# Kernel optimization log

Measured on AMD Instinct MI355X. Metric: run time of the kernel, lower is better.

The kernel has to match this reference:

```python
import jax, jax.numpy as jnp
import numpy as np

N = 50000    # nodes
E = 800000   # edges (avg degree 16)
B = 256      # graphs in the batch (static for segment ops)
H = 128      # feature / hidden width (channels[-2])
NL = 4       # LSTM layers in Set2Set
PS = 4       # Set2Set processing steps
OUT = 2      # channels[-1]


def _bn(h, g, b):
    # BatchNorm1d with batch statistics (training-mode math, biased variance)
    m = h.mean(0)
    v = jnp.mean((h - m) ** 2, 0)
    return (h - m) * jax.lax.rsqrt(v + 1e-5) * g + b


def _gin(x, src, dst, W1, b1, ga1, be1, W2, b2, ga2, be2):
    # GINConv, eps=0: out = MLP(x + sum_{j->i} x_j)
    agg = jax.ops.segment_sum(x[src], dst, num_segments=x.shape[0])
    h = x + agg
    h = jax.nn.relu(_bn(h @ W1.T + b1, ga1, be1))
    h = jax.nn.relu(_bn(h @ W2.T + b2, ga2, be2))
    return h


def _set2set(x, batch, Wih0, Whh0, b0, WihR, WhhR, bR):
    hs = [jnp.zeros((B, H), x.dtype)] * NL
    cs = [jnp.zeros((B, H), x.dtype)] * NL
    q_star = jnp.zeros((B, 2 * H), x.dtype)
    for _ in range(PS):
        inp = q_star
        nhs, ncs = [], []
        for l in range(NL):  # stacked LSTM cells, seq-len 1 per step
            Wih = Wih0 if l == 0 else WihR[l - 1]
            Whh = Whh0 if l == 0 else WhhR[l - 1]
            bb = b0 if l == 0 else bR[l - 1]
            gates = inp @ Wih.T + hs[l] @ Whh.T + bb
            i, f, g, o = jnp.split(gates, 4, axis=-1)  # torch gate order i,f,g,o
            c = jax.nn.sigmoid(f) * cs[l] + jax.nn.sigmoid(i) * jnp.tanh(g)
            h = jax.nn.sigmoid(o) * jnp.tanh(c)
            nhs.append(h); ncs.append(c)
            inp = h
        hs, cs = nhs, ncs
        q = inp  # (B, H) top-layer hidden
        # per-graph segment softmax attention
        e = jnp.sum(x * q[batch], -1)                        # (N,)
        m = jax.ops.segment_max(e, batch, num_segments=B)
        ee = jnp.exp(e - m[batch])
        s = jax.ops.segment_sum(ee, batch, num_segments=B)
        a = ee / s[batch]
        r = jax.ops.segment_sum(a[:, None] * x, batch, num_segments=B)  # (B, H)
        q_star = jnp.concatenate([q, r], -1)
    return q_star


def setup_inputs() -> dict:
    key = jax.random.key(0)
    ks = jax.random.split(key, 16)

    def w(k, shape):
        return jax.random.normal(k, shape, jnp.float32) * 0.05

    d = {}
    d["x"] = jax.random.normal(ks[0], (N, H), jnp.float32)
    d["edge_index"] = jax.random.randint(ks[1], (2, E), 0, N, dtype=jnp.int32)
    d["batch"] = jnp.sort(jax.random.randint(ks[2], (N,), 0, B, dtype=jnp.int32))
    for i, g in enumerate(("g0", "g1")):
        kk = jax.random.split(ks[3 + i], 2)
        d[g + "_W1"] = w(kk[0], (H, H)); d[g + "_b1"] = jnp.zeros((H,), jnp.float32)
        d[g + "_gamma1"] = jnp.ones((H,), jnp.float32); d[g + "_beta1"] = jnp.zeros((H,), jnp.float32)
        d[g + "_W2"] = w(kk[1], (H, H)); d[g + "_b2"] = jnp.zeros((H,), jnp.float32)
        d[g + "_gamma2"] = jnp.ones((H,), jnp.float32); d[g + "_beta2"] = jnp.zeros((H,), jnp.float32)
    d["Wih0"] = w(ks[6], (4 * H, 2 * H))
    d["Whh0"] = w(ks[7], (4 * H, H))
    d["b0"] = jnp.zeros((4 * H,), jnp.float32)
    d["WihR"] = w(ks[8], (NL - 1, 4 * H, H))
    d["WhhR"] = w(ks[9], (NL - 1, 4 * H, H))
    d["bR"] = jnp.zeros((NL - 1, 4 * H), jnp.float32)
    d["lin_W"] = w(ks[10], (OUT, 2 * H))
    d["lin_b"] = jnp.zeros((OUT,), jnp.float32)
    return d


def reference(x, edge_index, batch,
              g0_W1, g0_b1, g0_gamma1, g0_beta1, g0_W2, g0_b2, g0_gamma2, g0_beta2,
              g1_W1, g1_b1, g1_gamma1, g1_beta1, g1_W2, g1_b2, g1_gamma2, g1_beta2,
              Wih0, Whh0, b0, WihR, WhhR, bR, lin_W, lin_b):
    src, dst = edge_index[0], edge_index[1]
    x = _gin(x, src, dst, g0_W1, g0_b1, g0_gamma1, g0_beta1, g0_W2, g0_b2, g0_gamma2, g0_beta2)
    x = _gin(x, src, dst, g1_W1, g1_b1, g1_gamma1, g1_beta1, g1_W2, g1_b2, g1_gamma2, g1_beta2)
    q = _set2set(x, batch, Wih0, Whh0, b0, WihR, WhhR, bR)
    # F.dropout(p=0.1) is identity in eval mode
    return q @ lin_W.T + lin_b
```

## Files before the change

### kernel.cpp

```cpp
#include <hip/hip_runtime.h>
#include <math.h>

#define NN 50000
#define EE 800000
#define BBG 256
#define HHC 128
#define SEG_CAP 448
#define ESC 512
#define NBIN 196
#define NBLK 196

typedef _Float16 half8 __attribute__((ext_vector_type(8)));
typedef _Float16 half4 __attribute__((ext_vector_type(4)));
typedef _Float16 half2v __attribute__((ext_vector_type(2)));
typedef float f32x4 __attribute__((ext_vector_type(4)));

#if defined(__has_builtin)
#if __has_builtin(__builtin_amdgcn_fdot2)
#define USE_FDOT2 1
#endif
#endif

__device__ __forceinline__ float fdot2f(half2v a, half2v b, float c) {
#ifdef USE_FDOT2
  return __builtin_amdgcn_fdot2(a, b, c, false);
#else
  return fmaf((float)a[0], (float)b[0], fmaf((float)a[1], (float)b[1], c));
#endif
}

__device__ __forceinline__ float fsigm(float x) {
  return __builtin_amdgcn_rcpf(1.f + __expf(-x));
}
__device__ __forceinline__ float ftanh(float x) {
  return 1.f - 2.f * __builtin_amdgcn_rcpf(1.f + __expf(2.f * x));
}

__device__ __forceinline__ float4 aff4(float4 v, float4 sc, float4 sh) {
  v.x = fmaxf(fmaf(v.x, sc.x, sh.x), 0.f);
  v.y = fmaxf(fmaf(v.y, sc.y, sh.y), 0.f);
  v.z = fmaxf(fmaf(v.z, sc.z, sh.z), 0.f);
  v.w = fmaxf(fmaf(v.w, sc.w, sh.w), 0.f);
  return v;
}
__device__ __forceinline__ void add4(float4& a, float4 b) {
  a.x += b.x; a.y += b.y; a.z += b.z; a.w += b.w;
}
__device__ __forceinline__ float4 cvt4(half4 h) {
  return make_float4((float)h[0], (float)h[1], (float)h[2], (float)h[3]);
}

__global__ __launch_bounds__(256) void prep_all_kernel(
    const int* __restrict__ batch,
    const int* __restrict__ ei,
    const float* __restrict__ W0, const float* __restrict__ W1,
    const float* __restrict__ W2, const float* __restrict__ W3,
    const float* __restrict__ Wih0, const float* __restrict__ Whh0,
    const float* __restrict__ WihR, const float* __restrict__ WhhR,
    const float* __restrict__ b0, const float* __restrict__ bR,
    const float* __restrict__ xsrc,
    float* __restrict__ stats, int* __restrict__ gptr, int* __restrict__ partial,
    _Float16* __restrict__ ginWh, _Float16* __restrict__ WT0h,
    _Float16* __restrict__ WTRh, float* __restrict__ bc0, float* __restrict__ bcR,
    _Float16* __restrict__ x16a) {
  __shared__ int hist[NBIN];
  int blk = blockIdx.x, tid = threadIdx.x;
  if (blk == 0) {
    ((float4*)stats)[tid] = make_float4(0.f, 0.f, 0.f, 0.f);
    return;
  }
  if (blk <= 196) {
    int i = (blk - 1) * 256 + tid;
    if (i >= NN) return;
    int b = batch[i];
    int prev = (i == 0) ? -1 : batch[i - 1];
    for (int g = prev + 1; g <= b; ++g) gptr[g] = i;
    if (i == NN - 1) {
      for (int g = b + 1; g <= BBG; ++g) gptr[g] = NN;
    }
    return;
  }
  if (blk <= 392) {
    int b = blk - 197;
    if (tid < NBIN) hist[tid] = 0;
    __syncthreads();
    const int4* dst4 = (const int4*)(ei + EE);
#pragma unroll
    for (int c = 0; c < 4; ++c) {
      int idx = b * 1024 + c * 256 + tid;
      if (idx < EE / 4) {
        int4 d = dst4[idx];
        atomicAdd(&hist[d.x >> 8], 1);
        atomicAdd(&hist[d.y >> 8], 1);
        atomicAdd(&hist[d.z >> 8], 1);
        atomicAdd(&hist[d.w >> 8], 1);
      }
    }
    __syncthreads();
    if (tid < NBIN) partial[tid * NBLK + b] = hist[tid];
    return;
  }
  if (blk >= 2961) {
    int i = (blk - 2961) * 256 + tid;
    float4 v = ((const float4*)xsrc)[i];
    half4 h;
    h[0] = (_Float16)v.x; h[1] = (_Float16)v.y;
    h[2] = (_Float16)v.z; h[3] = (_Float16)v.w;
    ((half4*)x16a)[i] = h;
    return;
  }
  int idx = (blk - 393) * 256 + tid;
  if (idx < 65536) {
    int m = idx >> 14;
    int r = idx & 16383;
    const float* W = (m == 0) ? W0 : (m == 1) ? W1 : (m == 2) ? W2 : W3;
    ginWh[idx] = (_Float16)W[r];
  } else if (idx < 262144) {
    int t = idx - 65536;
    int k = t >> 9, op = t & 511;
    int j = op >> 2, g = op & 3;
    int row = g * 128 + j;
    float v = (k < 256) ? Wih0[row * 256 + k] : Whh0[row * 128 + (k - 256)];
    WT0h[((k >> 1) << 10) | (op << 1) | (k & 1)] = (_Float16)v;
  } else if (idx < 655360) {
    int t = idx - 262144;
    int l = t >> 17;
    int rem = t & 131071;
    int k = rem >> 9, op = rem & 511;
    int j = op >> 2, g = op & 3;
    int row = g * 128 + j;
    float v = (k < 128) ? WihR[((size_t)l * 512 + row) * 128 + k]
                        : WhhR[((size_t)l * 512 + row) * 128 + (k - 128)];
    WTRh[((size_t)l << 17) | ((k >> 1) << 10) | (op << 1) | (k & 1)] = (_Float16)v;
  } else {
    int t = idx - 655360;
    if (t < 512) {
      bc0[t] = b0[(t & 3) * 128 + (t >> 2)];
    } else {
      int u = t - 512;
      int l = u >> 9, op = u & 511;
      bcR[u] = bR[l * 512 + (op & 3) * 128 + (op >> 2)];
    }
  }
}


__global__ void scan_partials_kernel(const int* __restrict__ partial,
                                     int* __restrict__ block_base, int* __restrict__ total) {
  __shared__ int buf[256];
  int bin = blockIdx.x, tid = threadIdx.x;
  int v = (tid < NBLK) ? partial[bin * NBLK + tid] : 0;
  buf[tid] = v;
  __syncthreads();
  for (int off = 1; off < 256; off <<= 1) {
    int t = (tid >= off) ? buf[tid - off] : 0;
    __syncthreads();
    buf[tid] += t;
    __syncthreads();
  }
  if (tid < NBLK) block_base[bin * NBLK + tid] = buf[tid] - v;
  if (tid == 255) total[bin] = buf[255];
}

__global__ void scan_totals_kernel(const int* __restrict__ total, int* __restrict__ coarse_base) {
  __shared__ int buf[256];
  int tid = threadIdx.x;
  int v = (tid < NBIN) ? total[tid] : 0;
  buf[tid] = v;
  __syncthreads();
  for (int off = 1; off < 256; off <<= 1) {
    int t = (tid >= off) ? buf[tid - off] : 0;
    __syncthreads();
    buf[tid] += t;
    __syncthreads();
  }
  if (tid < NBIN) coarse_base[tid] = buf[tid] - v;
  if (tid == 255) coarse_base[NBIN] = buf[255];
}

__global__ __launch_bounds__(256) void bucket_scatter_kernel(const int* __restrict__ ei,
                                                             const int* __restrict__ coarse_base,
                                                             const int* __restrict__ block_base,
                                                             int* __restrict__ packed) {
  __shared__ int cursor[NBIN];
  int tid = threadIdx.x, b = blockIdx.x;
  if (tid < NBIN) cursor[tid] = coarse_base[tid] + block_base[tid * NBLK + b];
  __syncthreads();
  const int4* src4 = (const int4*)ei;
  const int4* dst4 = (const int4*)(ei + EE);
#pragma unroll
  for (int c = 0; c < 4; ++c) {
    int idx = b * 1024 + c * 256 + tid;
    if (idx < EE / 4) {
      int4 s = src4[idx];
      int4 d = dst4[idx];
      int p;
      p = atomicAdd(&cursor[d.x >> 8], 1); packed[p] = (s.x << 8) | (d.x & 255);
      p = atomicAdd(&cursor[d.y >> 8], 1); packed[p] = (s.y << 8) | (d.y & 255);
      p = atomicAdd(&cursor[d.z >> 8], 1); packed[p] = (s.z << 8) | (d.z & 255);
      p = atomicAdd(&cursor[d.w >> 8], 1); packed[p] = (s.w << 8) | (d.w & 255);
    }
  }
}

__global__ __launch_bounds__(256) void csr_finalize_kernel(const int* __restrict__ packed,
                                                           const int* __restrict__ coarse_base,
                                                           int* __restrict__ row_start,
                                                           int* __restrict__ csr) {
  __shared__ int fh[256];
  __shared__ int fb[256];
  int bin = blockIdx.x, tid = threadIdx.x;
  int e0 = coarse_base[bin], e1 = coarse_base[bin + 1];
  fh[tid] = 0;
  __syncthreads();
  for (int e = e0 + tid; e < e1; e += 256) atomicAdd(&fh[packed[e] & 255], 1);
  __syncthreads();
  int v = fh[tid];
  fb[tid] = v;
  __syncthreads();
  for (int off = 1; off < 256; off <<= 1) {
    int t = (tid >= off) ? fb[tid - off] : 0;
    __syncthreads();
    fb[tid] += t;
    __syncthreads();
  }
  int excl = fb[tid] - v;
  int node = bin * 256 + tid;
  if (node < NN) row_start[node] = e0 + excl;
  if (bin == NBIN - 1 && tid == 0) row_start[NN] = EE;
  __syncthreads();
  fb[tid] = excl;
  __syncthreads();
  for (int e = e0 + tid; e < e1; e += 256) {
    int p = packed[e];
    int pos = atomicAdd(&fb[p & 255], 1);
    csr[e0 + pos] = p >> 8;
  }
}


template <bool AFF>
__global__ __launch_bounds__(256) void gin_agg_kernel(
    const _Float16* __restrict__ x16, const int* __restrict__ row_start,
    const int* __restrict__ csr,
    const float* __restrict__ stats, const float* __restrict__ gamma,
    const float* __restrict__ beta, float* __restrict__ outp) {
  __shared__ float sc_s[128], sh_s[128];
  if (AFF) {
    int t = threadIdx.x;
    if (t < 128) {
      const float invN = 1.0f / (float)NN;
      float mm = stats[t] * invN;
      float vv = stats[128 + t] * invN - mm * mm;
      float rs = rsqrtf(vv + 1e-5f);
      float sc = gamma[t] * rs;
      sc_s[t] = sc;
      sh_s[t] = beta[t] - mm * sc;
    }
    __syncthreads();
  }
  int node = blockIdx.x * 4 + (threadIdx.x >> 6);
  int lane = threadIdx.x & 63;
  int half = lane >> 5, ln = lane & 31;
  const half4* xh = (const half4*)x16;
  float4 sc4 = make_float4(0.f, 0.f, 0.f, 0.f), sh4 = sc4;
  if (AFF) {
    sc4 = *(const float4*)&sc_s[4 * ln];
    sh4 = *(const float4*)&sh_s[4 * ln];
  }
  int s0 = row_start[node], s1 = row_start[node + 1];
  float4 self = cvt4(xh[(size_t)node * 32 + ln]);
  if (AFF) self = aff4(self, sc4, sh4);
  float4 c0 = make_float4(0.f, 0.f, 0.f, 0.f), c1 = c0, c2 = c0, c3 = c0;
  int cnt = s1 - s0;
  int mainEnd = s0 + (cnt & ~15);
  for (int j = s0; j < mainEnd; j += 16) {
    int i0 = csr[j + half + 0];
    int i1 = csr[j + half + 2];
    int i2 = csr[j + half + 4];
    int i3 = csr[j + half + 6];
    int i4 = csr[j + half + 8];
    int i5 = csr[j + half + 10];
    int i6 = csr[j + half + 12];
    int i7 = csr[j + half + 14];
    half4 h0 = xh[(size_t)i0 * 32 + ln];
    half4 h1 = xh[(size_t)i1 * 32 + ln];
    half4 h2 = xh[(size_t)i2 * 32 + ln];
    half4 h3 = xh[(size_t)i3 * 32 + ln];
    half4 h4 = xh[(size_t)i4 * 32 + ln];
    half4 h5 = xh[(size_t)i5 * 32 + ln];
    half4 h6 = xh[(size_t)i6 * 32 + ln];
    half4 h7 = xh[(size_t)i7 * 32 + ln];
    float4 v0 = cvt4(h0);
    float4 v1 = cvt4(h1);
    float4 v2 = cvt4(h2);
    float4 v3 = cvt4(h3);
    float4 v4 = cvt4(h4);
    float4 v5 = cvt4(h5);
    float4 v6 = cvt4(h6);
    float4 v7 = cvt4(h7);
    if (AFF) {
      v0 = aff4(v0, sc4, sh4); v1 = aff4(v1, sc4, sh4);
      v2 = aff4(v2, sc4, sh4); v3 = aff4(v3, sc4, sh4);
      v4 = aff4(v4, sc4, sh4); v5 = aff4(v5, sc4, sh4);
      v6 = aff4(v6, sc4, sh4); v7 = aff4(v7, sc4, sh4);
    }
    add4(c0, v0); add4(c1, v1); add4(c2, v2); add4(c3, v3);
    add4(c0, v4); add4(c1, v5); add4(c2, v6); add4(c3, v7);
  }
  for (int j = mainEnd + half; j < s1; j += 2) {
    int i = csr[j];
    float4 v = cvt4(xh[(size_t)i * 32 + ln]);
    if (AFF) v = aff4(v, sc4, sh4);
    add4(c0, v);
  }
  float4 t;
  t.x = (c0.x + c1.x) + (c2.x + c3.x);
  t.y = (c0.y + c1.y) + (c2.y + c3.y);
  t.z = (c0.z + c1.z) + (c2.z + c3.z);
  t.w = (c0.w + c1.w) + (c2.w + c3.w);
  t.x += __shfl_xor(t.x, 32);
  t.y += __shfl_xor(t.y, 32);
  t.z += __shfl_xor(t.z, 32);
  t.w += __shfl_xor(t.w, 32);
  t.x += self.x; t.y += self.y; t.z += self.z; t.w += self.w;
  if (half == 0) ((float4*)outp)[(size_t)node * 32 + ln] = t;
}

template <bool BN, bool AH>
__global__ __launch_bounds__(256) void gemm_gin_mfma_kernel(
    const float* __restrict__ A, const _Float16* __restrict__ A16,
    const _Float16* __restrict__ Wh,
    const float* __restrict__ bias,
    const float* __restrict__ stats, const float* __restrict__ gamma,
    const float* __restrict__ beta,
    float* __restrict__ C, _Float16* __restrict__ h16out,
    float* __restrict__ ssum, float* __restrict__ ssq) {
  __shared__ float bsc_s[128], bsh_s[128];
  int tid = threadIdx.x;
  if (BN) {
    if (tid < 128) {
      const float invN = 1.0f / (float)NN;
      float mm = stats[tid] * invN;
      float vv = stats[128 + tid] * invN - mm * mm;
      float rs = rsqrtf(vv + 1e-5f);
      float sc = gamma[tid] * rs;
      bsc_s[tid] = sc;
      bsh_s[tid] = beta[tid] - mm * sc;
    }
    __syncthreads();
  }
  int w = tid >> 6, l = tid & 63;
  int lr = l & 15, lg = l >> 4;
  int cb = w * 32;
  half8 bf0[4], bf1[4];
#pragma unroll
  for (int ks = 0; ks < 4; ++ks) {
    int k = ks * 32 + lg * 8;
    bf0[ks] = *(const half8*)(Wh + (size_t)(cb + lr) * 128 + k);
    bf1[ks] = *(const half8*)(Wh + (size_t)(cb + 16 + lr) * 128 + k);
  }
  float bv0 = bias[cb + lr], bv1 = bias[cb + 16 + lr];
  float ps0 = 0.f, pq0 = 0.f, ps1 = 0.f, pq1 = 0.f;
  int t0 = blockIdx.x * 4;
  for (int t = 0; t < 4; ++t) {
    int tile = t0 + t;
    if (tile >= 3125) break;
    int r = tile * 16 + lr;
    half8 af[4];
#pragma unroll
    for (int ks = 0; ks < 4; ++ks) {
      int k0 = ks * 32 + lg * 8;
      if constexpr (AH) {
        half8 ah = *(const half8*)(A16 + (size_t)r * 128 + k0);
        if constexpr (BN) {
          float4 s0 = *(const float4*)&bsc_s[k0];
          float4 s1 = *(const float4*)&bsc_s[k0 + 4];
          float4 h0 = *(const float4*)&bsh_s[k0];
          float4 h1 = *(const float4*)&bsh_s[k0 + 4];
          half8 o;
          o[0] = (_Float16)fmaxf(fmaf((float)ah[0], s0.x, h0.x), 0.f);
          o[1] = (_Float16)fmaxf(fmaf((float)ah[1], s0.y, h0.y), 0.f);
          o[2] = (_Float16)fmaxf(fmaf((float)ah[2], s0.z, h0.z), 0.f);
          o[3] = (_Float16)fmaxf(fmaf((float)ah[3], s0.w, h0.w), 0.f);
          o[4] = (_Float16)fmaxf(fmaf((float)ah[4], s1.x, h1.x), 0.f);
          o[5] = (_Float16)fmaxf(fmaf((float)ah[5], s1.y, h1.y), 0.f);
          o[6] = (_Float16)fmaxf(fmaf((float)ah[6], s1.z, h1.z), 0.f);
          o[7] = (_Float16)fmaxf(fmaf((float)ah[7], s1.w, h1.w), 0.f);
          af[ks] = o;
        } else {
          af[ks] = ah;
        }
      } else {
        float4 a0 = *(const float4*)(A + (size_t)r * 128 + k0);
        float4 a1 = *(const float4*)(A + (size_t)r * 128 + k0 + 4);
        if constexpr (BN) {
          float4 s0 = *(const float4*)&bsc_s[k0];
          float4 s1 = *(const float4*)&bsc_s[k0 + 4];
          float4 h0 = *(const float4*)&bsh_s[k0];
          float4 h1 = *(const float4*)&bsh_s[k0 + 4];
          a0 = aff4(a0, s0, h0);
          a1 = aff4(a1, s1, h1);
        }
        half8 o;
        o[0] = (_Float16)a0.x; o[1] = (_Float16)a0.y;
        o[2] = (_Float16)a0.z; o[3] = (_Float16)a0.w;
        o[4] = (_Float16)a1.x; o[5] = (_Float16)a1.y;
        o[6] = (_Float16)a1.z; o[7] = (_Float16)a1.w;
        af[ks] = o;
      }
    }
    f32x4 acc0 = {0.f, 0.f, 0.f, 0.f};
    f32x4 acc1 = {0.f, 0.f, 0.f, 0.f};
#pragma unroll
    for (int ks = 0; ks < 4; ++ks) {
      acc0 = __builtin_amdgcn_mfma_f32_16x16x32_f16(af[ks], bf0[ks], acc0, 0, 0, 0);
      acc1 = __builtin_amdgcn_mfma_f32_16x16x32_f16(af[ks], bf1[ks], acc1, 0, 0, 0);
    }
#pragma unroll
    for (int i = 0; i < 4; ++i) {
      int rr = tile * 16 + lg * 4 + i;
      float v0 = acc0[i] + bv0;
      float v1 = acc1[i] + bv1;
      if (C) {
        C[(size_t)rr * 128 + cb + lr] = v0;
        C[(size_t)rr * 128 + cb + 16 + lr] = v1;
      }
      if (h16out) {
        h16out[(size_t)rr * 128 + cb + lr] = (_Float16)v0;
        h16out[(size_t)rr * 128 + cb + 16 + lr] = (_Float16)v1;
      }
      ps0 += v0; pq0 += v0 * v0;
      ps1 += v1; pq1 += v1 * v1;
    }
  }
  ps0 += __shfl_xor(ps0, 16); ps0 += __shfl_xor(ps0, 32);
  pq0 += __shfl_xor(pq0, 16); pq0 += __shfl_xor(pq0, 32);
  ps1 += __shfl_xor(ps1, 16); ps1 += __shfl_xor(ps1, 32);
  pq1 += __shfl_xor(pq1, 16); pq1 += __shfl_xor(pq1, 32);
  if (lg == 0) {
    atomicAdd(&ssum[cb + lr], ps0);
    atomicAdd(&ssq[cb + lr], pq0);
    atomicAdd(&ssum[cb + 16 + lr], ps1);
    atomicAdd(&ssq[cb + 16 + lr], pq1);
  }
}

__global__ void __launch_bounds__(1024) set2set_kernel(
    const float* __restrict__ x, const int* __restrict__ gptr,
    const float* __restrict__ stats, const float* __restrict__ gamma,
    const float* __restrict__ beta,
    const _Float16* __restrict__ WT0h, const _Float16* __restrict__ WTRh,
    const float* __restrict__ bc0, const float* __restrict__ bcR,
    float* __restrict__ ebuf,
    const float* __restrict__ linW, const float* __restrict__ linb,
    float* __restrict__ out) {
  __shared__ half2v xs[SEG_CAP * 64];
  __shared__ float wpart[16][512];
  __shared__ float gates[512];
  __shared__ half2v inp2[192];
  __shared__ float hcs[4][128];
  __shared__ float ccs[4][128];
  __shared__ float qst[256];
  __shared__ float es[ESC];
  __shared__ float bsc[128], bsh[128];
  __shared__ float wred[16];
  __shared__ float smax_s, ssum_s;
  __shared__ float fred[2][4];

  int g = blockIdx.x, tid = threadIdx.x;
  int w16 = tid >> 6, lane = tid & 63;

  if (tid < 128) {
    const float invN = 1.0f / (float)NN;
    float mm = stats[tid] * invN;
    float vv = stats[128 + tid] * invN - mm * mm;
    float rs = rsqrtf(vv + 1e-5f);
    float sc = gamma[tid] * rs;
    bsc[tid] = sc;
    bsh[tid] = beta[tid] - mm * sc;
#pragma unroll
    for (int l = 0; l < 4; ++l) { hcs[l][tid] = 0.f; ccs[l][tid] = 0.f; }
  }
  if (tid < 256) qst[tid] = 0.f;
  __syncthreads();

  int s0 = gptr[g], s1 = gptr[g + 1];
  int seg = s1 - s0;
  int ncache = seg < SEG_CAP ? seg : SEG_CAP;
  const float2* x2 = (const float2*)x;
  float sc0 = bsc[2 * lane], sc1 = bsc[2 * lane + 1];
  float sh0 = bsh[2 * lane], sh1 = bsh[2 * lane + 1];
  for (int n = w16; n < ncache; n += 16) {
    float2 v = x2[(size_t)(s0 + n) * 64 + lane];
    half2v h;
    h[0] = (_Float16)fmaxf(fmaf(v.x, sc0, sh0), 0.f);
    h[1] = (_Float16)fmaxf(fmaf(v.y, sc1, sh1), 0.f);
    xs[n * 64 + lane] = h;
  }
  __syncthreads();

  int s_ = tid >> 6, cg = tid & 63;

  for (int step = 0; step < 4; ++step) {
    for (int cell = 0; cell < 4; ++cell) {
      const _Float16* WTh; const float* bias; int KP2;
      if (cell == 0) {
        WTh = WT0h; bias = bc0; KP2 = 12;
        if (tid < 192) {
          int k = tid << 1;
          float va, vb;
          if (k < 256) { va = qst[k]; vb = qst[k + 1]; }
          else { va = hcs[0][k - 256]; vb = hcs[0][k - 255]; }
          half2v h; h[0] = (_Float16)va; h[1] = (_Float16)vb;
          inp2[tid] = h;
        }
      } else {
        WTh = WTRh + (size_t)(cell - 1) * 131072;
        bias = bcR + (cell - 1) * 512; KP2 = 8;
        if (tid < 128) {
          int k = tid << 1;
          float va, vb;
          if (k < 128) { va = hcs[cell - 1][k]; vb = hcs[cell - 1][k + 1]; }
          else { va = hcs[cell][k - 128]; vb = hcs[cell][k - 127]; }
          half2v h; h[0] = (_Float16)va; h[1] = (_Float16)vb;
          inp2[tid] = h;
        }
      }
      __syncthreads();
      if (step == 0 && cell == 0) {
        if (tid < 512) gates[tid] = bias[tid];
        __syncthreads();
      } else {
        int se = (s_ + g) & 15;
        int k20 = se * KP2;
        float a0 = 0.f, a1 = 0.f, a2 = 0.f, a3 = 0.f;
        float a4 = 0.f, a5 = 0.f, a6 = 0.f, a7 = 0.f;
        if (step != 0 || se < 8) {
          const char* wb = (const char*)WTh + (size_t)k20 * 2048 + (cg << 5);
#pragma unroll 4
          for (int k2 = 0; k2 < KP2; ++k2) {
            uint4 wa = *(const uint4*)(wb + (size_t)k2 * 2048);
            uint4 wc = *(const uint4*)(wb + (size_t)k2 * 2048 + 16);
            half2v i2 = inp2[k20 + k2];
            a0 = fdot2f(i2, __builtin_bit_cast(half2v, wa.x), a0);
            a1 = fdot2f(i2, __builtin_bit_cast(half2v, wa.y), a1);
            a2 = fdot2f(i2, __builtin_bit_cast(half2v, wa.z), a2);
            a3 = fdot2f(i2, __builtin_bit_cast(half2v, wa.w), a3);
            a4 = fdot2f(i2, __builtin_bit_cast(half2v, wc.x), a4);
            a5 = fdot2f(i2, __builtin_bit_cast(half2v, wc.y), a5);
            a6 = fdot2f(i2, __builtin_bit_cast(half2v, wc.z), a6);
            a7 = fdot2f(i2, __builtin_bit_cast(half2v, wc.w), a7);
          }
        }
        *(float4*)&wpart[s_][cg << 3] = make_float4(a0, a1, a2, a3);
        *(float4*)(&wpart[s_][cg << 3] + 4) = make_float4(a4, a5, a6, a7);
        __syncthreads();
        if (tid < 512) {
          float acc = bias[tid];
#pragma unroll
          for (int s = 0; s < 16; ++s) acc += wpart[s][tid];
          gates[tid] = acc;
        }
        __syncthreads();
      }
      if (tid < 128) {
        int j = tid;
        float gi = gates[4 * j + 0];
        float gf = gates[4 * j + 1];
        float gc = gates[4 * j + 2];
        float go = gates[4 * j + 3];
        float cp = ccs[cell][j];
        float si = fsigm(gi);
        float sf = fsigm(gf);
        float so = fsigm(go);
        float cn = sf * cp + si * ftanh(gc);
        ccs[cell][j] = cn;
        hcs[cell][j] = so * ftanh(cn);
      }
      __syncthreads();
    }
    float* rpart = &wpart[0][0];
    float qx = hcs[3][2 * lane], qy = hcs[3][2 * lane + 1];
    half2v q2; q2[0] = (_Float16)qx; q2[1] = (_Float16)qy;
    float wmax = -3.0e38f;
    for (int n = w16; n < seg; n += 16) {
      float e;
      if (n < ncache) {
        e = fdot2f(xs[n * 64 + lane], q2, 0.f);
      } else {
        float2 v = x2[(size_t)(s0 + n) * 64 + lane];
        float vx = fmaxf(fmaf(v.x, sc0, sh0), 0.f);
        float vy = fmaxf(fmaf(v.y, sc1, sh1), 0.f);
        e = vx * qx + vy * qy;
      }
#pragma unroll
      for (int sh = 32; sh; sh >>= 1) e += __shfl_xor(e, sh);
      if (lane == 0) { if (n < ESC) es[n] = e; else ebuf[s0 + n] = e; }
      wmax = fmaxf(wmax, e);
    }
    if (lane == 0) wred[w16] = wmax;
    __syncthreads();
    if (tid == 0) {
      float m = wred[0];
#pragma unroll
      for (int t = 1; t < 16; ++t) m = fmaxf(m, wred[t]);
      smax_s = m;
    }
    __syncthreads();
    float m = smax_s;
    float loc = 0.f;
    for (int n = tid; n < seg; n += 1024) {
      float e = (n < ESC) ? es[n] : ebuf[s0 + n];
      float ex = __expf(e - m);
      if (n < ESC) es[n] = ex; else ebuf[s0 + n] = ex;
      loc += ex;
    }
#pragma unroll
    for (int sh = 32; sh; sh >>= 1) loc += __shfl_xor(loc, sh);
    __syncthreads();
    if (lane == 0) wred[w16] = loc;
    __syncthreads();
    if (tid == 0) {
      float s = 0.f;
#pragma unroll
      for (int t = 0; t < 16; ++t) s += wred[t];
      ssum_s = s;
    }
    __syncthreads();
    float inv = 1.0f / ssum_s;
    float rx = 0.f, ry = 0.f;
    for (int n = w16; n < seg; n += 16) {
      float ex = (n < ESC) ? es[n] : ebuf[s0 + n];
      float coef = ex * inv;
      float vx, vy;
      if (n < ncache) {
        half2v v2 = xs[n * 64 + lane];
        vx = (float)v2[0]; vy = (float)v2[1];
      } else {
        float2 v = x2[(size_t)(s0 + n) * 64 + lane];
        vx = fmaxf(fmaf(v.x, sc0, sh0), 0.f);
        vy = fmaxf(fmaf(v.y, sc1, sh1), 0.f);
      }
      rx += coef * vx; ry += coef * vy;
    }
    rpart[w16 * 128 + 2 * lane] = rx;
    rpart[w16 * 128 + 2 * lane + 1] = ry;
    __syncthreads();
    if (tid < 128) {
      float r = 0.f;
#pragma unroll
      for (int t = 0; t < 16; ++t) r += rpart[t * 128 + tid];
      qst[tid] = hcs[3][tid];
      qst[128 + tid] = r;
    }
    __syncthreads();
  }
  if (tid < 256) {
    float val = qst[tid];
    float p0 = val * linW[tid];
    float p1 = val * linW[256 + tid];
#pragma unroll
    for (int sh = 32; sh; sh >>= 1) { p0 += __shfl_xor(p0, sh); p1 += __shfl_xor(p1, sh); }
    if (lane == 0) { fred[0][w16] = p0; fred[1][w16] = p1; }
  }
  __syncthreads();
  if (tid == 0) {
    out[2 * g + 0] = fred[0][0] + fred[0][1] + fred[0][2] + fred[0][3] + linb[0];
    out[2 * g + 1] = fred[1][0] + fred[1][1] + fred[1][2] + fred[1][3] + linb[1];
  }
}


extern "C" void kernel_launch(void* const* d_in, const int* in_sizes, int n_in,
                              void* d_out, int out_size, void* d_ws, size_t ws_size,
                              hipStream_t stream) {
  const float* x = (const float*)d_in[0];
  const int* ei = (const int*)d_in[1];
  const int* batch = (const int*)d_in[2];
  const float* gW[4]  = {(const float*)d_in[3],  (const float*)d_in[7],
                         (const float*)d_in[11], (const float*)d_in[15]};
  const float* gb[4]  = {(const float*)d_in[4],  (const float*)d_in[8],
                         (const float*)d_in[12], (const float*)d_in[16]};
  const float* gga[4] = {(const float*)d_in[5],  (const float*)d_in[9],
                         (const float*)d_in[13], (const float*)d_in[17]};
  const float* gbe[4] = {(const float*)d_in[6],  (const float*)d_in[10],
                         (const float*)d_in[14], (const float*)d_in[18]};
  const float* Wih0 = (const float*)d_in[19];
  const float* Whh0 = (const float*)d_in[20];
  const float* b0   = (const float*)d_in[21];
  const float* WihR = (const float*)d_in[22];
  const float* WhhR = (const float*)d_in[23];
  const float* bR   = (const float*)d_in[24];
  const float* linW = (const float*)d_in[25];
  const float* linb = (const float*)d_in[26];
  float* out = (float*)d_out;

  char* base = (char*)d_ws;
  size_t off = 0;
  auto allocf = [&](size_t n) { float* p = (float*)(base + off); off += n * sizeof(float); return p; };
  float* xa    = allocf(6400000);
  float* xb    = allocf(6400000);
  _Float16* ginWh = (_Float16*)(base + off); off += 65536 * 2;
  _Float16* WT0h = (_Float16*)(base + off); off += 196608 * 2;
  _Float16* WTRh = (_Float16*)(base + off); off += 393216 * 2;
  _Float16* x16a = (_Float16*)(base + off); off += 6400000 * 2;
  _Float16* x16b = (_Float16*)(base + off); off += 6400000 * 2;
  float* bc0   = allocf(512);
  float* bcR   = allocf(1536);
  float* ebuf  = allocf(50000);
  float* stats = allocf(1024);
  int* row_start = (int*)(base + off); off += 50004 * 4;
  int* gptr = (int*)(base + off); off += 260 * 4;
  int* csr = (int*)(base + off); off += 800000 * 4;
  int* packed = (int*)(base + off); off += 800000 * 4;
  int* partial = (int*)(base + off); off += NBIN * NBLK * 4;
  int* block_base = (int*)(base + off); off += NBIN * NBLK * 4;
  int* total = (int*)(base + off); off += 256 * 4;
  int* coarse_base = (int*)(base + off); off += 260 * 4;
  (void)ws_size; (void)in_sizes; (void)n_in; (void)out_size;

  prep_all_kernel<<<9211, 256, 0, stream>>>(batch, ei, gW[0], gW[1], gW[2], gW[3],
                                            Wih0, Whh0, WihR, WhhR, b0, bR, x,
                                            stats, gptr, partial, ginWh, WT0h, WTRh,
                                            bc0, bcR, x16a);
  scan_partials_kernel<<<NBIN, 256, 0, stream>>>(partial, block_base, total);
  scan_totals_kernel<<<1, 256, 0, stream>>>(total, coarse_base);
  bucket_scatter_kernel<<<NBLK, 256, 0, stream>>>(ei, coarse_base, block_base, packed);
  csr_finalize_kernel<<<NBIN, 256, 0, stream>>>(packed, coarse_base, row_start, csr);

  gin_agg_kernel<false><<<12500, 256, 0, stream>>>(x16a, row_start, csr,
                                                   nullptr, nullptr, nullptr, xb);
  gemm_gin_mfma_kernel<false, false><<<782, 256, 0, stream>>>(
      xb, nullptr, ginWh + 0 * 16384, gb[0],
      nullptr, nullptr, nullptr,
      nullptr, x16a, stats + 0, stats + 128);
  gemm_gin_mfma_kernel<true, true><<<782, 256, 0, stream>>>(
      nullptr, x16a, ginWh + 1 * 16384, gb[1],
      stats + 0, gga[0], gbe[0],
      nullptr, x16b, stats + 256, stats + 384);
  gin_agg_kernel<true><<<12500, 256, 0, stream>>>(x16b, row_start, csr,
                                                  stats + 256, gga[1], gbe[1], xa);
  gemm_gin_mfma_kernel<false, false><<<782, 256, 0, stream>>>(
      xa, nullptr, ginWh + 2 * 16384, gb[2],
      nullptr, nullptr, nullptr,
      nullptr, x16a, stats + 512, stats + 640);
  gemm_gin_mfma_kernel<true, true><<<782, 256, 0, stream>>>(
      nullptr, x16a, ginWh + 3 * 16384, gb[3],
      stats + 512, gga[2], gbe[2],
      xa, nullptr, stats + 768, stats + 896);

  set2set_kernel<<<256, 1024, 0, stream>>>(xa, gptr, stats + 768, gga[3], gbe[3],
                                           WT0h, WTRh, bc0, bcR, ebuf, linW, linb, out);
}
```

Before: 442.9 us.

## Store GIN aggregation in fp16 with 16-byte gathers and fuse LSTM gate reduction

The neighbour aggregation kernel now has each lane load half8 (16 bytes) per neighbour, with four edge groups per wavefront reduced by shuffles. Its output is written as fp16 instead of fp32, and the following GEMM reads that fp16 buffer directly through its half-precision input path. This halves the write and read traffic of the aggregated features and cuts the number of load instructions. In set2set, the separate gate-reduction pass and its barrier are folded into the cell-update threads. The cost is an extra fp16 rounding of the aggregated sums, which lowers precision.

```diff
diff --git a/kernel.cpp b/kernel.cpp
--- a/kernel.cpp
+++ b/kernel.cpp
@@ -42,12 +42,6 @@
   v.z = fmaxf(fmaf(v.z, sc.z, sh.z), 0.f);
   v.w = fmaxf(fmaf(v.w, sc.w, sh.w), 0.f);
   return v;
-}
-__device__ __forceinline__ void add4(float4& a, float4 b) {
-  a.x += b.x; a.y += b.y; a.z += b.z; a.w += b.w;
-}
-__device__ __forceinline__ float4 cvt4(half4 h) {
-  return make_float4((float)h[0], (float)h[1], (float)h[2], (float)h[3]);
 }
 
 __global__ __launch_bounds__(256) void prep_all_kernel(
@@ -238,93 +232,90 @@
   }
 }
 
-
 template <bool AFF>
 __global__ __launch_bounds__(256) void gin_agg_kernel(
     const _Float16* __restrict__ x16, const int* __restrict__ row_start,
     const int* __restrict__ csr,
     const float* __restrict__ stats, const float* __restrict__ gamma,
-    const float* __restrict__ beta, float* __restrict__ outp) {
+    const float* __restrict__ beta, _Float16* __restrict__ outp) {
   __shared__ float sc_s[128], sh_s[128];
   if (AFF) {
-    int t = threadIdx.x;
-    if (t < 128) {
+    int tt = threadIdx.x;
+    if (tt < 128) {
       const float invN = 1.0f / (float)NN;
-      float mm = stats[t] * invN;
-      float vv = stats[128 + t] * invN - mm * mm;
+      float mm = stats[tt] * invN;
+      float vv = stats[128 + tt] * invN - mm * mm;
       float rs = rsqrtf(vv + 1e-5f);
-      float sc = gamma[t] * rs;
-      sc_s[t] = sc;
-      sh_s[t] = beta[t] - mm * sc;
+      float sc = gamma[tt] * rs;
+      sc_s[tt] = sc;
+      sh_s[tt] = beta[tt] - mm * sc;
     }
     __syncthreads();
   }
   int node = blockIdx.x * 4 + (threadIdx.x >> 6);
   int lane = threadIdx.x & 63;
-  int half = lane >> 5, ln = lane & 31;
-  const half4* xh = (const half4*)x16;
-  float4 sc4 = make_float4(0.f, 0.f, 0.f, 0.f), sh4 = sc4;
+  int q = lane >> 4, t = lane & 15;
+  const half8* xh8 = (const half8*)x16;
+  float scv[8], shv[8];
   if (AFF) {
-    sc4 = *(const float4*)&sc_s[4 * ln];
-    sh4 = *(const float4*)&sh_s[4 * ln];
+#pragma unroll
+    for (int f = 0; f < 8; ++f) { scv[f] = sc_s[t * 8 + f]; shv[f] = sh_s[t * 8 + f]; }
   }
   int s0 = row_start[node], s1 = row_start[node + 1];
-  float4 self = cvt4(xh[(size_t)node * 32 + ln]);
-  if (AFF) self = aff4(self, sc4, sh4);
-  float4 c0 = make_float4(0.f, 0.f, 0.f, 0.f), c1 = c0, c2 = c0, c3 = c0;
+  float acc[8] = {0.f, 0.f, 0.f, 0.f, 0.f, 0.f, 0.f, 0.f};
   int cnt = s1 - s0;
   int mainEnd = s0 + (cnt & ~15);
   for (int j = s0; j < mainEnd; j += 16) {
-    int i0 = csr[j + half + 0];
-    int i1 = csr[j + half + 2];
-    int i2 = csr[j + half + 4];
-    int i3 = csr[j + half + 6];
-    int i4 = csr[j + half + 8];
-    int i5 = csr[j + half + 10];
-    int i6 = csr[j + half + 12];
-    int i7 = csr[j + half + 14];
-    half4 h0 = xh[(size_t)i0 * 32 + ln];
-    half4 h1 = xh[(size_t)i1 * 32 + ln];
-    half4 h2 = xh[(size_t)i2 * 32 + ln];
-    half4 h3 = xh[(size_t)i3 * 32 + ln];
-    half4 h4 = xh[(size_t)i4 * 32 + ln];
-    half4 h5 = xh[(size_t)i5 * 32 + ln];
-    half4 h6 = xh[(size_t)i6 * 32 + ln];
-    half4 h7 = xh[(size_t)i7 * 32 + ln];
-    float4 v0 = cvt4(h0);
-    float4 v1 = cvt4(h1);
-    float4 v2 = cvt4(h2);
-    float4 v3 = cvt4(h3);
-    float4 v4 = cvt4(h4);
-    float4 v5 = cvt4(h5);
-    float4 v6 = cvt4(h6);
-    float4 v7 = cvt4(h7);
+    int i0 = csr[j + q + 0];
+    int i1 = csr[j + q + 4];
+    int i2 = csr[j + q + 8];
+    int i3 = csr[j + q + 12];
+    half8 h0 = xh8[(size_t)i0 * 16 + t];
+    half8 h1 = xh8[(size_t)i1 * 16 + t];
+    half8 h2 = xh8[(size_t)i2 * 16 + t];
+    half8 h3 = xh8[(size_t)i3 * 16 + t];
     if (AFF) {
-      v0 = aff4(v0, sc4, sh4); v1 = aff4(v1, sc4, sh4);
-      v2 = aff4(v2, sc4, sh4); v3 = aff4(v3, sc4, sh4);
-      v4 = aff4(v4, sc4, sh4); v5 = aff4(v5, sc4, sh4);
-      v6 = aff4(v6, sc4, sh4); v7 = aff4(v7, sc4, sh4);
-    }
-    add4(c0, v0); add4(c1, v1); add4(c2, v2); add4(c3, v3);
-    add4(c0, v4); add4(c1, v5); add4(c2, v6); add4(c3, v7);
-  }
-  for (int j = mainEnd + half; j < s1; j += 2) {
+#pragma unroll
+      for (int f = 0; f < 8; ++f) {
+        acc[f] += fmaxf(fmaf((float)h0[f], scv[f], shv[f]), 0.f);
+        acc[f] += fmaxf(fmaf((float)h1[f], scv[f], shv[f]), 0.f);
+        acc[f] += fmaxf(fmaf((float)h2[f], scv[f], shv[f]), 0.f);
+        acc[f] += fmaxf(fmaf((float)h3[f], scv[f], shv[f]), 0.f);
+      }
+    } else {
+#pragma unroll
+      for (int f = 0; f < 8; ++f) {
+        acc[f] += ((float)h0[f] + (float)h1[f]) + ((float)h2[f] + (float)h3[f]);
+      }
+    }
+  }
+  for (int j = mainEnd + q; j < s1; j += 4) {
     int i = csr[j];
-    float4 v = cvt4(xh[(size_t)i * 32 + ln]);
-    if (AFF) v = aff4(v, sc4, sh4);
-    add4(c0, v);
-  }
-  float4 t;
-  t.x = (c0.x + c1.x) + (c2.x + c3.x);
-  t.y = (c0.y + c1.y) + (c2.y + c3.y);
-  t.z = (c0.z + c1.z) + (c2.z + c3.z);
-  t.w = (c0.w + c1.w) + (c2.w + c3.w);
-  t.x += __shfl_xor(t.x, 32);
-  t.y += __shfl_xor(t.y, 32);
-  t.z += __shfl_xor(t.z, 32);
-  t.w += __shfl_xor(t.w, 32);
-  t.x += self.x; t.y += self.y; t.z += self.z; t.w += self.w;
-  if (half == 0) ((float4*)outp)[(size_t)node * 32 + ln] = t;
+    half8 h = xh8[(size_t)i * 16 + t];
+    if (AFF) {
+#pragma unroll
+      for (int f = 0; f < 8; ++f) acc[f] += fmaxf(fmaf((float)h[f], scv[f], shv[f]), 0.f);
+    } else {
+#pragma unroll
+      for (int f = 0; f < 8; ++f) acc[f] += (float)h[f];
+    }
+  }
+#pragma unroll
+  for (int f = 0; f < 8; ++f) {
+    acc[f] += __shfl_xor(acc[f], 16);
+    acc[f] += __shfl_xor(acc[f], 32);
+  }
+  if (q == 0) {
+    half8 selfh = xh8[(size_t)node * 16 + t];
+    half8 hv;
+#pragma unroll
+    for (int f = 0; f < 8; ++f) {
+      float sv = (float)selfh[f];
+      if (AFF) sv = fmaxf(fmaf(sv, scv[f], shv[f]), 0.f);
+      hv[f] = (_Float16)(acc[f] + sv);
+    }
+    ((half8*)outp)[(size_t)node * 16 + t] = hv;
+  }
 }
 
 template <bool BN, bool AH>
@@ -457,7 +448,6 @@
     float* __restrict__ out) {
   __shared__ half2v xs[SEG_CAP * 64];
   __shared__ float wpart[16][512];
-  __shared__ float gates[512];
   __shared__ half2v inp2[192];
   __shared__ float hcs[4][128];
   __shared__ float ccs[4][128];
@@ -528,10 +518,8 @@
         }
       }
       __syncthreads();
-      if (step == 0 && cell == 0) {
-        if (tid < 512) gates[tid] = bias[tid];
-        __syncthreads();
-      } else {
+      bool skipmv = (step == 0 && cell == 0);
+      if (!skipmv) {
         int se = (s_ + g) & 15;
         int k20 = se * KP2;
         float a0 = 0.f, a1 = 0.f, a2 = 0.f, a3 = 0.f;
@@ -556,25 +544,22 @@
         *(float4*)&wpart[s_][cg << 3] = make_float4(a0, a1, a2, a3);
         *(float4*)(&wpart[s_][cg << 3] + 4) = make_float4(a4, a5, a6, a7);
         __syncthreads();
-        if (tid < 512) {
-          float acc = bias[tid];
-#pragma unroll
-          for (int s = 0; s < 16; ++s) acc += wpart[s][tid];
-          gates[tid] = acc;
-        }
-        __syncthreads();
       }
       if (tid < 128) {
         int j = tid;
-        float gi = gates[4 * j + 0];
-        float gf = gates[4 * j + 1];
-        float gc = gates[4 * j + 2];
-        float go = gates[4 * j + 3];
+        float4 ga = *(const float4*)&bias[4 * j];
+        if (!skipmv) {
+#pragma unroll
+          for (int s = 0; s < 16; ++s) {
+            float4 wv = *(const float4*)&wpart[s][4 * j];
+            ga.x += wv.x; ga.y += wv.y; ga.z += wv.z; ga.w += wv.w;
+          }
+        }
         float cp = ccs[cell][j];
-        float si = fsigm(gi);
-        float sf = fsigm(gf);
-        float so = fsigm(go);
-        float cn = sf * cp + si * ftanh(gc);
+        float si = fsigm(ga.x);
+        float sf = fsigm(ga.y);
+        float so = fsigm(ga.w);
+        float cn = sf * cp + si * ftanh(ga.z);
         ccs[cell][j] = cn;
         hcs[cell][j] = so * ftanh(cn);
       }
@@ -700,7 +685,7 @@
   size_t off = 0;
   auto allocf = [&](size_t n) { float* p = (float*)(base + off); off += n * sizeof(float); return p; };
   float* xa    = allocf(6400000);
-  float* xb    = allocf(6400000);
+  _Float16* agg16 = (_Float16*)(base + off); off += 6400000 * 2;
   _Float16* ginWh = (_Float16*)(base + off); off += 65536 * 2;
   _Float16* WT0h = (_Float16*)(base + off); off += 196608 * 2;
   _Float16* WTRh = (_Float16*)(base + off); off += 393216 * 2;
@@ -730,9 +715,9 @@
   csr_finalize_kernel<<<NBIN, 256, 0, stream>>>(packed, coarse_base, row_start, csr);
 
   gin_agg_kernel<false><<<12500, 256, 0, stream>>>(x16a, row_start, csr,
-                                                   nullptr, nullptr, nullptr, xb);
-  gemm_gin_mfma_kernel<false, false><<<782, 256, 0, stream>>>(
-      xb, nullptr, ginWh + 0 * 16384, gb[0],
+                                                   nullptr, nullptr, nullptr, agg16);
+  gemm_gin_mfma_kernel<false, true><<<782, 256, 0, stream>>>(
+      nullptr, agg16, ginWh + 0 * 16384, gb[0],
       nullptr, nullptr, nullptr,
       nullptr, x16a, stats + 0, stats + 128);
   gemm_gin_mfma_kernel<true, true><<<782, 256, 0, stream>>>(
@@ -740,9 +725,9 @@
       stats + 0, gga[0], gbe[0],
       nullptr, x16b, stats + 256, stats + 384);
   gin_agg_kernel<true><<<12500, 256, 0, stream>>>(x16b, row_start, csr,
-                                                  stats + 256, gga[1], gbe[1], xa);
-  gemm_gin_mfma_kernel<false, false><<<782, 256, 0, stream>>>(
-      xa, nullptr, ginWh + 2 * 16384, gb[2],
+                                                  stats + 256, gga[1], gbe[1], agg16);
+  gemm_gin_mfma_kernel<false, true><<<782, 256, 0, stream>>>(
+      nullptr, agg16, ginWh + 2 * 16384, gb[2],
       nullptr, nullptr, nullptr,
       nullptr, x16a, stats + 512, stats + 640);
   gemm_gin_mfma_kernel<true, true><<<782, 256, 0, stream>>>(
```

Result: faster. 425.4 us (-3.9%).
